# Kernel optimization log

Hardware: AMD Instinct MI355X
Metric: run time of the kernel (lower is better)

## Reference

```python
import jax, jax.numpy as jnp
import numpy as np

# ViT-B on the Lorentz hyperboloid (curvature C): points x = [x_time, x_space],
# x_time = sqrt(||x_space||^2 + C). All linear/conv/norm ops act on the space
# part and recompute time; residuals/attention-midpoints renormalize the full
# Lorentz vector back onto the hyperboloid.
B, IMG, P, CIN, D, H, L = 32, 224, 16, 3, 768, 12, 12
HD = D // H          # per-head space dim (64)
DFF = 2048           # swiglu hidden: int(2/3 * 4*768) aligned to 64
C = 1.0
EPS = 1e-6


def _time(xs):
    return jnp.sqrt(jnp.clip(jnp.sum(xs * xs, -1, keepdims=True) + C, EPS, None))


def _to_lorentz(xs):
    return jnp.concatenate([_time(xs), xs], -1)


def _project(z):
    # renormalize full Lorentz vector so <z,z>_L = -C
    zz = jnp.sum(z[..., 1:] ** 2, -1, keepdims=True) - z[..., :1] ** 2
    return z * (jnp.sqrt(C) / jnp.sqrt(jnp.clip(-zz, EPS, None)))


def _lorentz_ln(x, g, b):
    xs = x[..., 1:]
    mu = xs.mean(-1, keepdims=True)
    var = ((xs - mu) ** 2).mean(-1, keepdims=True)
    xs = (xs - mu) / jnp.sqrt(var + 1e-6) * g + b
    return _to_lorentz(xs)


def _lresnet(x, y, w):
    # Lorentzian weighted residual: midpoint of x and w*y, projected to manifold
    return _project(x + w * y)


def _rope_tables():
    # 2D axial rope over the 14x14 patch grid, identity rotation for 1 cls token
    n = IMG // P
    d4 = HD // 4
    inv = 1.0 / (100.0 ** (np.arange(d4) / d4))
    ang = np.arange(n)[:, None] * inv[None, :]            # [n, d4]
    ay = np.repeat(ang[:, None, :], n, axis=1)            # row angles
    ax = np.repeat(ang[None, :, :], n, axis=0)            # col angles
    a = np.concatenate([ay, ax], -1).reshape(n * n, HD // 2)
    cos = np.concatenate([np.ones((1, HD // 2)), np.cos(a)], 0)
    sin = np.concatenate([np.zeros((1, HD // 2)), np.sin(a)], 0)
    return jnp.asarray(cos, jnp.float32), jnp.asarray(sin, jnp.float32)


def _apply_rope(x, cos, sin):
    # x: [B,N,H,HD]; rotate consecutive pairs (complex multiply)
    xr = x.reshape(*x.shape[:-1], -1, 2)
    x0, x1 = xr[..., 0], xr[..., 1]
    c = cos[None, :, None, :]
    s = sin[None, :, None, :]
    out = jnp.stack([x0 * c - x1 * s, x0 * s + x1 * c], -1)
    return out.reshape(x.shape)


def _attention(x, Wq, Wk, Wv, Wo, cos, sin, scale):
    b, n, _ = x.shape
    xs = x[..., 1:]
    q = (xs @ Wq).reshape(b, n, H, HD)
    k = (xs @ Wk).reshape(b, n, H, HD)
    v = (xs @ Wv).reshape(b, n, H, HD)
    q = _apply_rope(q, cos, sin)
    k = _apply_rope(k, cos, sin)
    qt = _time(q)[..., 0]   # [B,N,H]
    kt = _time(k)[..., 0]
    # Lorentz inner product <q,k>_L = -q_t k_t + q_s . k_s
    inner = jnp.einsum('bnhd,bmhd->bhnm', q, k) - jnp.einsum('bnh,bmh->bhnm', qt, kt)
    attn = jax.nn.softmax((2.0 * C + 2.0 * inner) / scale, axis=-1)
    vf = jnp.concatenate([_time(v), v], -1)               # [B,M,H,HD+1]
    mid = jnp.einsum('bhnm,bmhe->bnhe', attn, vf)         # Lorentzian midpoint
    mid = _project(mid)
    out_s = mid[..., 1:].reshape(b, n, H * HD) @ Wo       # concat heads + proj
    return _to_lorentz(out_s)


def setup_inputs() -> dict:
    key = jax.random.key(0)
    ks = jax.random.split(key, 12)
    std = 0.02
    nrm = lambda k, shape: jax.random.normal(k, shape, jnp.float32) * std
    return {
        'x': jax.random.normal(ks[0], (B, CIN, IMG, IMG), jnp.float32),
        'cls_s': nrm(ks[1], (D - 1,)),
        'Wp': nrm(ks[2], (P, P, CIN + 1, D - 1)),         # HWIO conv kernel
        'ln1_g': jnp.ones((L, D - 1), jnp.float32),
        'ln1_b': jnp.zeros((L, D - 1), jnp.float32),
        'Wq': nrm(ks[3], (L, D - 1, H * HD)),
        'Wk': nrm(ks[4], (L, D - 1, H * HD)),
        'Wv': nrm(ks[5], (L, D - 1, H * HD)),
        'Wo': nrm(ks[6], (L, H * HD, D - 1)),
        'ln2_g': jnp.ones((L, D - 1), jnp.float32),
        'ln2_b': jnp.zeros((L, D - 1), jnp.float32),
        'W1': nrm(ks[7], (L, D - 1, DFF)),
        'W2': nrm(ks[8], (L, D - 1, DFF)),
        'W3': nrm(ks[9], (L, DFF, D - 1)),
        'wy1': jnp.ones((L,), jnp.float32),
        'wy2': jnp.ones((L,), jnp.float32),
        'lnf_g': jnp.ones((D - 1,), jnp.float32),
        'lnf_b': jnp.zeros((D - 1,), jnp.float32),
    }


def reference(x, cls_s, Wp, ln1_g, ln1_b, Wq, Wk, Wv, Wo, ln2_g, ln2_b,
              W1, W2, W3, wy1, wy2, lnf_g, lnf_b):
    b = x.shape[0]
    xs = jnp.transpose(x, (0, 2, 3, 1))                   # BHWC
    xl = _to_lorentz(xs)                                  # pixel-wise time channel
    feat = jax.lax.conv_general_dilated(
        xl, Wp, (P, P), 'VALID',
        dimension_numbers=('NHWC', 'HWIO', 'NHWC'))       # [B,14,14,D-1]
    tok = _to_lorentz(feat).reshape(b, -1, D)             # [B,196,D]
    cls = jnp.broadcast_to(_to_lorentz(cls_s)[None, None, :], (b, 1, D))
    tok = jnp.concatenate([cls, tok], 1)                  # [B,197,D]
    cos, sin = _rope_tables()
    scale = jnp.sqrt(jnp.asarray(H * HD, jnp.float32))
    for l in range(L):
        xn = _lorentz_ln(tok, ln1_g[l], ln1_b[l])
        a = _attention(xn, Wq[l], Wk[l], Wv[l], Wo[l], cos, sin, scale)
        tok = _lresnet(tok, a, wy1[l])
        xn = _lorentz_ln(tok, ln2_g[l], ln2_b[l])
        hs = xn[..., 1:]
        m = _to_lorentz((jax.nn.silu(hs @ W1[l]) * (hs @ W2[l])) @ W3[l])
        tok = _lresnet(tok, m, wy2[l])
    return _lorentz_ln(tok, lnf_g, lnf_b)
```

## Files before the change

kernel.cpp:

```cpp
#include <hip/hip_runtime.h>
#include <hip/hip_bf16.h>

typedef __attribute__((ext_vector_type(8))) short short8;
typedef __attribute__((ext_vector_type(4))) float f32x4;
typedef _Float16 f16x8 __attribute__((ext_vector_type(8)));

#define NLAYER 12
#define NTOK   6304
#define MPAD   6400
#define CONVM  6272

#define QELE     ((size_t)384*208*64)
#define VELE     ((size_t)384*80*232)

#define WS_QKV ((size_t)2304*768)
#define WS_WO  ((size_t)768*768)
#define WS_W12 ((size_t)4096*768)
#define WS_W3  ((size_t)768*2048)

static constexpr size_t AL(size_t x){ return (x + 511) & ~(size_t)511; }
static constexpr size_t B_COS    = 0;
static constexpr size_t B_SIN    = AL(B_COS    + (size_t)197*32*4);
static constexpr size_t B_WPT    = AL(B_SIN    + (size_t)197*32*4);
static constexpr size_t B_APATCH = AL(B_WPT    + (size_t)768*1024*2);
static constexpr size_t B_WQKVT  = AL(B_APATCH + (size_t)CONVM*1024*2);
static constexpr size_t B_WOT    = AL(B_WQKVT  + WS_QKV*NLAYER*2);
static constexpr size_t B_W12T   = AL(B_WOT    + WS_WO*NLAYER*2);
static constexpr size_t B_W3T    = AL(B_W12T   + WS_W12*NLAYER*2);
static constexpr size_t B_TOK    = AL(B_W3T    + WS_W3*NLAYER*2);
static constexpr size_t B_ACTA   = AL(B_TOK    + (size_t)NTOK*768*4);
static constexpr size_t B_ACTB   = AL(B_ACTA   + (size_t)MPAD*768*2);
static constexpr size_t B_GOUT   = AL(B_ACTB   + (size_t)MPAD*2048*2);
static constexpr size_t B_QB     = AL(B_GOUT   + (size_t)MPAD*768*4);
static constexpr size_t B_KB     = AL(B_QB     + QELE*2);
static constexpr size_t B_VT     = AL(B_KB     + QELE*2);
static constexpr size_t B_QTB    = AL(B_VT     + VELE*2);
static constexpr size_t B_KTB    = AL(B_QTB    + (size_t)384*208*4);
static constexpr size_t B_END    = AL(B_KTB    + (size_t)384*208*4);

typedef __attribute__((address_space(1))) unsigned int gu32;
typedef __attribute__((address_space(3))) unsigned int lu32;
__device__ __forceinline__ void gld16(const void* g, void* l) {
  __builtin_amdgcn_global_load_lds((const gu32*)g, (lu32*)l, 16, 0, 0);
}

__device__ __forceinline__ float bsum(float v, float* red) {
  #pragma unroll
  for (int m = 32; m; m >>= 1) v += __shfl_xor(v, m, 64);
  __syncthreads();
  if ((threadIdx.x & 63) == 0) red[threadIdx.x >> 6] = v;
  __syncthreads();
  return red[0] + red[1] + red[2] + red[3];
}

__device__ __forceinline__ ushort h_us(float v) {
  _Float16 h = (_Float16)v;
  return *(ushort*)&h;
}
__device__ __forceinline__ float us_f(ushort u) {
  return (float)*(const _Float16*)&u;
}

__device__ __forceinline__ void xcd_remap(int& bx, int& by) {
  int gx = gridDim.x, gy = gridDim.y;
  int nwg = gx * gy;
  int orig = blockIdx.y * gx + blockIdx.x;
  int q = nwg >> 3, r = nwg & 7;
  int xcd = orig & 7, loc = orig >> 3;
  int wg = (xcd < r ? xcd * (q + 1) : r * (q + 1) + (xcd - r) * q) + loc;
  bx = wg / gy;
  by = wg % gy;
}

__global__ void k_rope_tab(float* __restrict__ cosb, float* __restrict__ sinb) {
  int idx = blockIdx.x * 256 + threadIdx.x;
  if (idx >= 197 * 32) return;
  int p = idx >> 5, j = idx & 31;
  float cv, sv;
  if (p == 0) { cv = 1.f; sv = 0.f; }
  else {
    int pp = p - 1;
    int iy = pp / 14, ix = pp - iy * 14;
    int pos = (j < 16) ? iy : ix;
    int f   = (j < 16) ? j  : j - 16;
    float inv = powf(100.f, -(float)f / 16.f);
    float a = (float)pos * inv;
    cv = cosf(a); sv = sinf(a);
  }
  cosb[idx] = cv; sinb[idx] = sv;
}

__device__ __forceinline__ void tpose_tile(const float* __restrict__ src, ushort* __restrict__ dst,
                                           int K, int N, int ldd, int imode, int tk, int tn) {
  __shared__ float ts[32][33];
  int t = threadIdx.x;
  int rr = t >> 3, c4 = (t & 7) * 4;
  int k0 = tk * 32, n0 = tn * 32;
  #pragma unroll
  for (int e = 0; e < 4; ++e) {
    int k = k0 + rr, n = n0 + c4 + e;
    ts[rr][c4 + e] = (k < K && n < N) ? src[(size_t)k * N + n] : 0.f;
  }
  __syncthreads();
  int c = n0 + rr;
  int drow = (imode == 0) ? c : (16 * (c >> 3) + (c & 7) + (imode == 2 ? 8 : 0));
  ushort4 o;
  #pragma unroll
  for (int e = 0; e < 4; ++e) {
    _Float16 hv = (_Float16)ts[c4 + e][rr];
    ((ushort*)&o)[e] = *(ushort*)&hv;
  }
  *(ushort4*)&dst[(size_t)drow * ldd + k0 + c4] = o;
}

__global__ __launch_bounds__(256) void k_tpose(const float* __restrict__ src, ushort* __restrict__ dst,
                                               int K, int N, int ktiles, int ldd) {
  int tk = blockIdx.x % ktiles, tn = blockIdx.x / ktiles;
  tpose_tile(src, dst, K, N, ldd, 0, tk, tn);
}

__global__ __launch_bounds__(256) void k_wprep12(const float* __restrict__ Wq, const float* __restrict__ Wk,
                                                 const float* __restrict__ Wv, const float* __restrict__ Wo,
                                                 const float* __restrict__ W1, const float* __restrict__ W2,
                                                 const float* __restrict__ W3,
                                                 ushort* __restrict__ wqkvt, ushort* __restrict__ wot,
                                                 ushort* __restrict__ w12t, ushort* __restrict__ w3t) {
  int gt = blockIdx.x;
  int l = gt / 6912;
  int tile = gt - l * 6912;
  const float* q  = Wq + (size_t)l * 767 * 768;
  const float* kk = Wk + (size_t)l * 767 * 768;
  const float* v  = Wv + (size_t)l * 767 * 768;
  const float* o  = Wo + (size_t)l * 768 * 767;
  const float* w1 = W1 + (size_t)l * 767 * 2048;
  const float* w2 = W2 + (size_t)l * 767 * 2048;
  const float* w3 = W3 + (size_t)l * 2048 * 767;
  ushort* dqkv = wqkvt + (size_t)l * WS_QKV;
  ushort* dwo  = wot   + (size_t)l * WS_WO;
  ushort* dw12 = w12t  + (size_t)l * WS_W12;
  ushort* dw3  = w3t   + (size_t)l * WS_W3;
  const float* src; ushort* dst;
  int K, N, ktiles, ldd, imode = 0, tl;
  if (tile < 2304) {
    int jb = tile / 576; tl = tile % 576;
    ktiles = 24; ldd = 768;
    if (jb == 0)      { src = q;  dst = dqkv;                 K = 767; N = 768; }
    else if (jb == 1) { src = kk; dst = dqkv + 768 * 768;     K = 767; N = 768; }
    else if (jb == 2) { src = v;  dst = dqkv + 2 * 768 * 768; K = 767; N = 768; }
    else              { src = o;  dst = dwo;                  K = 768; N = 767; }
  } else if (tile < 5376) {
    int jb = (tile - 2304) / 1536; tl = (tile - 2304) % 1536;
    ktiles = 24; ldd = 768; K = 767; N = 2048; dst = dw12;
    src = jb ? w2 : w1; imode = jb ? 2 : 1;
  } else {
    tl = tile - 5376; ktiles = 64; ldd = 2048; K = 2048; N = 767; src = w3; dst = dw3;
  }
  int tk = tl % ktiles, tn = tl / ktiles;
  tpose_tile(src, dst, K, N, ldd, imode, tk, tn);
}

__global__ __launch_bounds__(256) void k_im2col(const float* __restrict__ x, ushort* __restrict__ ap) {
  int r = blockIdx.x;
  int b = r / 196, pi = r - b * 196;
  int py = pi / 14, px = pi - py * 14;
  int t = threadIdx.x;
  int ph = t >> 4, pw = t & 15;
  int iy = py * 16 + ph, ix = px * 16 + pw;
  size_t base = ((size_t)b * 3 * 224 + iy) * 224 + ix;
  float x0 = x[base];
  float x1 = x[base + 224 * 224];
  float x2 = x[base + 2 * 224 * 224];
  float tv = sqrtf(fmaxf(x0 * x0 + x1 * x1 + x2 * x2 + 1.f, 1e-6f));
  size_t o = (size_t)r * 1024 + t * 4;
  ap[o] = h_us(tv); ap[o + 1] = h_us(x0); ap[o + 2] = h_us(x1); ap[o + 3] = h_us(x2);
}

template<int MODE>
__global__ __launch_bounds__(256) void k_gemmh(const ushort* __restrict__ A, const ushort* __restrict__ Bt,
                                               float* __restrict__ C, ushort* __restrict__ H,
                                               int N, int K) {
  __shared__ ushort sA[2][128 * 64];
  __shared__ ushort sB[2][128 * 64];
  int bx, by;
  xcd_remap(bx, by);
  int m0 = bx * 128, n0 = by * 128;
  int t = threadIdx.x;
  int w = t >> 6, l = t & 63;
  int wm = (w >> 1) * 64, wn = (w & 1) * 64;
  int lr = l & 15, hi = l >> 4;

  auto stage = [&](int k0, int buf) {
    #pragma unroll
    for (int i = 0; i < 4; ++i) {
      int fl = i * 256 + t;
      int r = fl >> 3, c = fl & 7;
      int cs = c ^ (r & 7);
      gld16(&A[(size_t)(m0 + r) * K + k0 + cs * 8], &sA[buf][fl * 8]);
      gld16(&Bt[(size_t)(n0 + r) * K + k0 + cs * 8], &sB[buf][fl * 8]);
    }
  };

  f32x4 acc[4][4] = {};
  stage(0, 0);
  __syncthreads();
  int buf = 0;
  for (int k0 = 0; k0 < K; k0 += 64) {
    if (k0 + 64 < K) stage(k0 + 64, buf ^ 1);
    f16x8 af[4][2], bfr[4][2];
    #pragma unroll
    for (int q = 0; q < 4; ++q) {
      int ra = wm + q * 16 + lr, rb = wn + q * 16 + lr;
      #pragma unroll
      for (int h = 0; h < 2; ++h) {
        af[q][h]  = *(const f16x8*)&sA[buf][ra * 64 + ((h * 4 + hi) ^ (ra & 7)) * 8];
        bfr[q][h] = *(const f16x8*)&sB[buf][rb * 64 + ((h * 4 + hi) ^ (rb & 7)) * 8];
      }
    }
    #pragma unroll
    for (int mi = 0; mi < 4; ++mi)
      #pragma unroll
      for (int ni = 0; ni < 4; ++ni) {
        acc[mi][ni] = __builtin_amdgcn_mfma_f32_16x16x32_f16(af[mi][0], bfr[ni][0], acc[mi][ni], 0, 0, 0);
        acc[mi][ni] = __builtin_amdgcn_mfma_f32_16x16x32_f16(af[mi][1], bfr[ni][1], acc[mi][ni], 0, 0, 0);
      }
    __syncthreads();
    buf ^= 1;
  }

  int rr = hi * 4, cc = lr;
  if (MODE == 1) {
    #pragma unroll
    for (int mi = 0; mi < 4; ++mi)
      #pragma unroll
      for (int ni = 0; ni < 4; ++ni) {
        int g = (n0 + wn + ni * 16) >> 4;
        #pragma unroll
        for (int j = 0; j < 4; ++j) {
          float v = acc[mi][ni][j];
          float p = __shfl_xor(v, 8);
          float u1 = (cc < 8) ? v : p;
          float u2 = (cc < 8) ? p : v;
          float hv = u1 / (1.f + __expf(-u1)) * u2;
          if (cc < 8)
            H[(size_t)(m0 + wm + mi * 16 + rr + j) * 2048 + g * 8 + cc] = h_us(hv);
        }
      }
  } else if (MODE == 3) {
    #pragma unroll
    for (int mi = 0; mi < 4; ++mi)
      #pragma unroll
      for (int ni = 0; ni < 4; ++ni)
        #pragma unroll
        for (int j = 0; j < 4; ++j)
          H[(size_t)(m0 + wm + mi * 16 + rr + j) * N + (n0 + wn + ni * 16 + cc)] = h_us(acc[mi][ni][j]);
  } else {
    #pragma unroll
    for (int mi = 0; mi < 4; ++mi)
      #pragma unroll
      for (int ni = 0; ni < 4; ++ni)
        #pragma unroll
        for (int j = 0; j < 4; ++j)
          C[(size_t)(m0 + wm + mi * 16 + rr + j) * N + (n0 + wn + ni * 16 + cc)] = acc[mi][ni][j];
  }
}

template<int MODE>
__global__ __launch_bounds__(512, 2) void k_g256(const ushort* __restrict__ A, const ushort* __restrict__ Bt,
                                                 ushort* __restrict__ H, int N, int K,
                                                 ushort* __restrict__ qbuf, ushort* __restrict__ kbuf,
                                                 ushort* __restrict__ vtb,
                                                 float* __restrict__ qtb, float* __restrict__ ktb,
                                                 const float* __restrict__ cosb, const float* __restrict__ sinb) {
  __shared__ ushort sA[2][2][256 * 32];
  __shared__ ushort sB[2][2][256 * 32];
  const int t = threadIdx.x;
  const int w = t >> 6, l = t & 63;
  const int wr = w >> 2, wc = w & 3;
  const int lr = l & 15, hi4 = l >> 4;
  int bx, by;
  xcd_remap(bx, by);
  const int m0 = bx * 256, n0 = by * 256;

  auto stageA = [&](int kt, int kh, int buf) {
    #pragma unroll
    for (int ii = 0; ii < 2; ++ii) {
      int q = ii * 512 + t;
      int r = q >> 2, ci = q & 3;
      gld16(&A[(size_t)(m0 + r) * K + kt * 64 + kh * 32 + ((ci ^ ((r >> 1) & 3)) * 8)], &sA[buf][kh][q * 8]);
    }
  };
  auto stageB = [&](int kt, int kh, int buf) {
    #pragma unroll
    for (int ii = 0; ii < 2; ++ii) {
      int q = ii * 512 + t;
      int r = q >> 2, ci = q & 3;
      gld16(&Bt[(size_t)(n0 + r) * K + kt * 64 + kh * 32 + ((ci ^ ((r >> 1) & 3)) * 8)], &sB[buf][kh][q * 8]);
    }
  };

  f32x4 acc[8][4] = {};
  auto ldA = [&](int buf, int ks, int G, f16x8* fr) {
    #pragma unroll
    for (int mi = 0; mi < 4; ++mi) {
      int r = wr * 128 + (G * 4 + mi) * 16 + lr;
      fr[mi] = *(const f16x8*)&sA[buf][ks][(r * 4 + (hi4 ^ ((r >> 1) & 3))) * 8];
    }
  };
  auto ldB = [&](int buf, int ks, f16x8* fr) {
    #pragma unroll
    for (int ni = 0; ni < 4; ++ni) {
      int r = wc * 64 + ni * 16 + lr;
      fr[ni] = *(const f16x8*)&sB[buf][ks][(r * 4 + (hi4 ^ ((r >> 1) & 3))) * 8];
    }
  };
  auto mmaG = [&](int G, f16x8* a, f16x8* b) {
    __builtin_amdgcn_s_setprio(1);
    #pragma unroll
    for (int mi = 0; mi < 4; ++mi)
      #pragma unroll
      for (int ni = 0; ni < 4; ++ni)
        acc[G * 4 + mi][ni] = __builtin_amdgcn_mfma_f32_16x16x32_f16(a[mi], b[ni], acc[G * 4 + mi][ni], 0, 0, 0);
    __builtin_amdgcn_s_setprio(0);
  };

  const int NT = K >> 6;
  const int NI = NT >> 1;
  stageA(0, 0, 0); stageB(0, 0, 0); stageA(0, 1, 0); stageB(0, 1, 0);

  for (int i = 0; i < NI; ++i) {
    const int T1 = 2 * i + 1, T2 = 2 * i + 2;
    const bool last = (i == NI - 1);
    f16x8 a0[4], a1[4], b0[4], b1[4];
    asm volatile("s_waitcnt vmcnt(4)" ::: "memory");
    __builtin_amdgcn_sched_barrier(0);
    __builtin_amdgcn_s_barrier();
    ldA(0, 0, 0, a0); ldB(0, 0, b0);
    stageA(T1, 0, 1);
    mmaG(0, a0, b0);
    ldA(0, 0, 1, a1);
    stageB(T1, 0, 1);
    mmaG(1, a1, b0);
    asm volatile("s_waitcnt vmcnt(4)" ::: "memory");
    __builtin_amdgcn_sched_barrier(0);
    __builtin_amdgcn_s_barrier();
    ldA(0, 1, 0, a0); ldB(0, 1, b1);
    stageA(T1, 1, 1);
    mmaG(0, a0, b1);
    ldA(0, 1, 1, a1);
    stageB(T1, 1, 1);
    mmaG(1, a1, b1);
    asm volatile("s_waitcnt vmcnt(4)" ::: "memory");
    __builtin_amdgcn_sched_barrier(0);
    __builtin_amdgcn_s_barrier();
    ldA(1, 0, 0, a0); ldB(1, 0, b0);
    if (!last) stageA(T2, 0, 0);
    mmaG(0, a0, b0);
    ldA(1, 0, 1, a1);
    if (!last) stageB(T2, 0, 0);
    mmaG(1, a1, b0);
    if (last) { asm volatile("s_waitcnt vmcnt(0)" ::: "memory"); }
    else      { asm volatile("s_waitcnt vmcnt(4)" ::: "memory"); }
    __builtin_amdgcn_sched_barrier(0);
    __builtin_amdgcn_s_barrier();
    ldA(1, 1, 0, a0); ldB(1, 1, b1);
    if (!last) stageA(T2, 1, 0);
    mmaG(0, a0, b1);
    ldA(1, 1, 1, a1);
    if (!last) stageB(T2, 1, 0);
    mmaG(1, a1, b1);
  }

  if (MODE == 2) {
    int secBase = n0 + wc * 64;
    int sec = secBase / 768;
    int hh = (secBase - sec * 768) >> 6;
    #pragma unroll
    for (int mi = 0; mi < 8; ++mi) {
      float nrm[4];
      #pragma unroll
      for (int j = 0; j < 4; ++j) {
        float ss = 0.f;
        #pragma unroll
        for (int ni = 0; ni < 4; ++ni) ss += acc[mi][ni][j] * acc[mi][ni][j];
        #pragma unroll
        for (int m = 8; m; m >>= 1) ss += __shfl_xor(ss, m, 64);
        nrm[j] = sqrtf(fmaxf(ss + 1.f, 1e-6f));
      }
      #pragma unroll
      for (int j = 0; j < 4; ++j) {
        int m = m0 + wr * 128 + mi * 16 + hi4 * 4 + j;
        if (m < NTOK) {
          int b = m / 197, nn = m - b * 197;
          int bh = b * 12 + hh;
          if (sec == 2) {
            size_t vo = (size_t)bh * 80 * 232;
            if (lr == 0) vtb[vo + nn] = h_us(nrm[j]);
            #pragma unroll
            for (int ni = 0; ni < 4; ++ni) {
              int e = ni * 16 + lr;
              vtb[vo + (size_t)(1 + e) * 232 + nn] = h_us(acc[mi][ni][j]);
            }
          } else {
            float* tb = (sec == 0) ? qtb : ktb;
            ushort* ob = (sec == 0) ? qbuf : kbuf;
            if (lr == 0) tb[(size_t)bh * 208 + nn] = nrm[j];
            size_t rowb = ((size_t)bh * 208 + nn) * 64;
            #pragma unroll
            for (int ni = 0; ni < 4; ++ni) {
              int d = ni * 16 + lr;
              float v = acc[mi][ni][j];
              float p = __shfl_xor(v, 1);
              int j2 = d >> 1;
              float cz = cosb[nn * 32 + j2], sz = sinb[nn * 32 + j2];
              float rv = ((lr & 1) == 0) ? (v * cz - p * sz) : (p * sz + v * cz);
              ob[rowb + d] = h_us(rv);
            }
          }
        }
      }
    }
  }
}

__global__ __launch_bounds__(256) void k_build_tok(const float* __restrict__ feat, const float* __restrict__ cls,
                                                   float* __restrict__ tok) {
  __shared__ float red[8];
  int r = blockIdx.x;
  int b = r / 197, i = r - b * 197;
  int t = threadIdx.x;
  const float* src = (i == 0) ? cls : (feat + (size_t)(b * 196 + i - 1) * 768);
  float v0 = src[t], v1 = src[256 + t], v2 = (t < 255) ? src[512 + t] : 0.f;
  float qs = bsum(v0 * v0 + v1 * v1 + v2 * v2, red);
  float* tp = tok + (size_t)r * 768;
  if (t == 0) tp[0] = sqrtf(fmaxf(qs + 1.f, 1e-6f));
  tp[1 + t] = v0; tp[257 + t] = v1; if (t < 255) tp[513 + t] = v2;
}

__global__ __launch_bounds__(256) void k_ln(const float* __restrict__ tok, const float* __restrict__ g,
                                            const float* __restrict__ bb, ushort* __restrict__ out) {
  __shared__ float red[8];
  int r = blockIdx.x, t = threadIdx.x;
  const float* xp = tok + (size_t)r * 768;
  float v0 = xp[1 + t], v1 = xp[257 + t], v2 = (t < 255) ? xp[513 + t] : 0.f;
  float s = bsum(v0 + v1 + v2, red);
  float q = bsum(v0 * v0 + v1 * v1 + v2 * v2, red);
  float mu = s * (1.f / 767.f);
  float rstd = rsqrtf(fmaxf(q * (1.f / 767.f) - mu * mu, 0.f) + 1e-6f);
  size_t o = (size_t)r * 768;
  out[o + t]       = h_us((v0 - mu) * rstd * g[t]       + bb[t]);
  out[o + 256 + t] = h_us((v1 - mu) * rstd * g[256 + t] + bb[256 + t]);
  if (t < 255)
    out[o + 512 + t] = h_us((v2 - mu) * rstd * g[512 + t] + bb[512 + t]);
  if (t == 255) out[o + 767] = 0;
}

__global__ __launch_bounds__(128) void k_attn(const ushort* __restrict__ qbuf,
                                              const float* __restrict__ qtb,
                                              const ushort* __restrict__ kbuf,
                                              const float* __restrict__ ktb,
                                              const ushort* __restrict__ vtb,
                                              ushort* __restrict__ outa) {
  __shared__ ushort sP[2][16 * 248];
  int bxt = blockIdx.x, bh = blockIdx.y;
  int b = bh / 12, hd = bh - b * 12;
  int t = threadIdx.x, w = t >> 6, l = t & 63;
  int rt = bxt * 2 + w;
  if (rt >= 13) return;
  int lr = l & 15, hi4 = l >> 4;
  const ushort* qg = qbuf + (size_t)bh * 208 * 64;
  const ushort* kg = kbuf + (size_t)bh * 208 * 64;
  const ushort* vg = vtb + (size_t)bh * 80 * 232;
  const float*  ktp = ktb + (size_t)bh * 208;
  const float invs = 0.03608439182435161f;
  ushort* pw = &sP[w][0];

  int qrow = (rt * 16 + lr) * 64 + hi4 * 8;
  f16x8 q0 = *(const f16x8*)&qg[qrow];
  f16x8 q1 = *(const f16x8*)&qg[qrow + 32];
  float qt4[4];
  #pragma unroll
  for (int j = 0; j < 4; ++j) qt4[j] = qtb[(size_t)bh * 208 + rt * 16 + hi4 * 4 + j];
  f32x4 acc[13];
  #pragma unroll
  for (int nt = 0; nt < 13; ++nt) {
    int kr = (nt * 16 + lr) * 64 + hi4 * 8;
    f16x8 k0 = *(const f16x8*)&kg[kr];
    f16x8 k1 = *(const f16x8*)&kg[kr + 32];
    acc[nt] = (f32x4){0.f, 0.f, 0.f, 0.f};
    acc[nt] = __builtin_amdgcn_mfma_f32_16x16x32_f16(q0, k0, acc[nt], 0, 0, 0);
    acc[nt] = __builtin_amdgcn_mfma_f32_16x16x32_f16(q1, k1, acc[nt], 0, 0, 0);
  }
  float mx[4] = {-1e30f, -1e30f, -1e30f, -1e30f};
  #pragma unroll
  for (int nt = 0; nt < 13; ++nt) {
    int cI = nt * 16 + lr;
    float ktc = ktp[cI];
    bool valid = (cI < 197);
    #pragma unroll
    for (int j = 0; j < 4; ++j) {
      float s = (2.f + 2.f * (acc[nt][j] - qt4[j] * ktc)) * invs;
      acc[nt][j] = s;
      if (valid) mx[j] = fmaxf(mx[j], s);
    }
  }
  #pragma unroll
  for (int j = 0; j < 4; ++j)
    #pragma unroll
    for (int m = 8; m; m >>= 1) mx[j] = fmaxf(mx[j], __shfl_xor(mx[j], m, 64));
  #pragma unroll
  for (int nt = 0; nt < 14; ++nt) {
    int cI = nt * 16 + lr;
    #pragma unroll
    for (int j = 0; j < 4; ++j) {
      float p = (nt < 13 && cI < 197) ? __expf(acc[nt][j] - mx[j]) : 0.f;
      pw[(hi4 * 4 + j) * 248 + cI] = h_us(p);
    }
  }
  f32x4 accO[5];
  #pragma unroll
  for (int et = 0; et < 5; ++et) accO[et] = (f32x4){0.f, 0.f, 0.f, 0.f};
  #pragma unroll
  for (int ks = 0; ks < 7; ++ks) {
    f16x8 pa = *(const f16x8*)&pw[lr * 248 + ks * 32 + hi4 * 8];
    #pragma unroll
    for (int et = 0; et < 5; ++et) {
      int er = et * 16 + lr;
      f16x8 bv = *(const f16x8*)&vg[(er > 64 ? 64 : er) * 232 + ks * 32 + hi4 * 8];
      accO[et] = __builtin_amdgcn_mfma_f32_16x16x32_f16(pa, bv, accO[et], 0, 0, 0);
    }
  }
  float ssq[4] = {0.f, 0.f, 0.f, 0.f};
  #pragma unroll
  for (int et = 0; et < 4; ++et)
    #pragma unroll
    for (int j = 0; j < 4; ++j) ssq[j] += accO[et][j] * accO[et][j];
  if (lr == 0) {
    #pragma unroll
    for (int j = 0; j < 4; ++j) ssq[j] += accO[4][j] * accO[4][j];
  }
  #pragma unroll
  for (int j = 0; j < 4; ++j)
    #pragma unroll
    for (int m = 8; m; m >>= 1) ssq[j] += __shfl_xor(ssq[j], m, 64);
  float rf4[4];
  #pragma unroll
  for (int j = 0; j < 4; ++j) {
    float o0 = __shfl(accO[0][j], (l & 48));
    rf4[j] = rsqrtf(fmaxf(2.f * o0 * o0 - ssq[j], 1e-6f));
  }
  #pragma unroll
  for (int et = 0; et < 5; ++et) {
    int e = et * 16 + lr;
    if (e == 0 || e >= 65) continue;
    #pragma unroll
    for (int j = 0; j < 4; ++j) {
      int n = rt * 16 + hi4 * 4 + j;
      if (n < 197)
        outa[((size_t)(b * 197 + n)) * 768 + hd * 64 + (e - 1)] = h_us(accO[et][j] * rf4[j]);
    }
  }
}

template<int FIN>
__global__ __launch_bounds__(256) void k_resnet_ln(float* __restrict__ tok, const ushort* __restrict__ s,
                                                   const float* __restrict__ wyp, int l,
                                                   const float* __restrict__ g, const float* __restrict__ bb,
                                                   ushort* __restrict__ out16, float* __restrict__ out32) {
  __shared__ float red[8];
  __shared__ float bc[1];
  int r = blockIdx.x, t = threadIdx.x;
  float w = wyp[l];
  const ushort* sp = s + (size_t)r * 768;
  float* tp = tok + (size_t)r * 768;
  float s0 = us_f(sp[t]), s1 = us_f(sp[256 + t]), s2 = (t < 255) ? us_f(sp[512 + t]) : 0.f;
  float qs = bsum(s0 * s0 + s1 * s1 + s2 * s2, red);
  float at = sqrtf(fmaxf(qs + 1.f, 1e-6f));
  float z0 = tp[1 + t] + w * s0;
  float z1 = tp[257 + t] + w * s1;
  float z2 = (t < 255) ? (tp[513 + t] + w * s2) : 0.f;
  float zs = bsum(z0 * z0 + z1 * z1 + z2 * z2, red);
  if (t == 0) bc[0] = tp[0] + w * at;
  __syncthreads();
  float zt = bc[0];
  float rf = rsqrtf(fmaxf(zt * zt - zs, 1e-6f));
  float n0 = z0 * rf, n1 = z1 * rf, n2 = z2 * rf;
  tp[1 + t] = n0; tp[257 + t] = n1; if (t < 255) tp[513 + t] = n2;
  if (t == 0) tp[0] = zt * rf;
  float sm = bsum(n0 + n1 + n2, red);
  float sq = bsum(n0 * n0 + n1 * n1 + n2 * n2, red);
  float mu = sm * (1.f / 767.f);
  float rstd = rsqrtf(fmaxf(sq * (1.f / 767.f) - mu * mu, 0.f) + 1e-6f);
  float y0 = (n0 - mu) * rstd * g[t] + bb[t];
  float y1 = (n1 - mu) * rstd * g[256 + t] + bb[256 + t];
  float y2 = (t < 255) ? ((n2 - mu) * rstd * g[512 + t] + bb[512 + t]) : 0.f;
  if (FIN) {
    float qq = bsum(y0 * y0 + y1 * y1 + y2 * y2, red);
    float* op = out32 + (size_t)r * 768;
    op[1 + t] = y0; op[257 + t] = y1; if (t < 255) op[513 + t] = y2;
    if (t == 0) op[0] = sqrtf(fmaxf(qq + 1.f, 1e-6f));
  } else {
    size_t o = (size_t)r * 768;
    out16[o + t] = h_us(y0);
    out16[o + 256 + t] = h_us(y1);
    if (t < 255) out16[o + 512 + t] = h_us(y2);
    if (t == 255) out16[o + 767] = 0;
  }
}

extern "C" void kernel_launch(void* const* d_in, const int* in_sizes, int n_in,
                              void* d_out, int out_size, void* d_ws, size_t ws_size,
                              hipStream_t stream) {
  const float* x     = (const float*)d_in[0];
  const float* cls_s = (const float*)d_in[1];
  const float* Wp    = (const float*)d_in[2];
  const float* ln1g  = (const float*)d_in[3];
  const float* ln1b  = (const float*)d_in[4];
  const float* Wq    = (const float*)d_in[5];
  const float* Wk    = (const float*)d_in[6];
  const float* Wv    = (const float*)d_in[7];
  const float* Wo    = (const float*)d_in[8];
  const float* ln2g  = (const float*)d_in[9];
  const float* ln2b  = (const float*)d_in[10];
  const float* W1    = (const float*)d_in[11];
  const float* W2    = (const float*)d_in[12];
  const float* W3    = (const float*)d_in[13];
  const float* wy1   = (const float*)d_in[14];
  const float* wy2   = (const float*)d_in[15];
  const float* lnfg  = (const float*)d_in[16];
  const float* lnfb  = (const float*)d_in[17];

  if (ws_size < B_END) return;

  char* ws = (char*)d_ws;
  float*  cosb   = (float*)(ws + B_COS);
  float*  sinb   = (float*)(ws + B_SIN);
  ushort* wpt    = (ushort*)(ws + B_WPT);
  ushort* apatch = (ushort*)(ws + B_APATCH);
  ushort* wqkvt  = (ushort*)(ws + B_WQKVT);
  ushort* wot    = (ushort*)(ws + B_WOT);
  ushort* w12t   = (ushort*)(ws + B_W12T);
  ushort* w3t    = (ushort*)(ws + B_W3T);
  float*  tok    = (float*)(ws + B_TOK);
  ushort* acta   = (ushort*)(ws + B_ACTA);
  ushort* actb   = (ushort*)(ws + B_ACTB);
  float*  gout   = (float*)(ws + B_GOUT);
  ushort* gouth  = (ushort*)(ws + B_GOUT);
  ushort* qbuf   = (ushort*)(ws + B_QB);
  ushort* kbuf   = (ushort*)(ws + B_KB);
  ushort* vtb    = (ushort*)(ws + B_VT);
  float*  qtb    = (float*)(ws + B_QTB);
  float*  ktb    = (float*)(ws + B_KTB);

  hipMemsetAsync(vtb, 0, VELE * 2, stream);

  k_rope_tab<<<25, 256, 0, stream>>>(cosb, sinb);
  k_tpose<<<32 * 24, 256, 0, stream>>>(Wp, wpt, 1024, 767, 32, 1024);
  k_im2col<<<CONVM, 256, 0, stream>>>(x, apatch);
  k_wprep12<<<6912 * NLAYER, 256, 0, stream>>>(Wq, Wk, Wv, Wo, W1, W2, W3, wqkvt, wot, w12t, w3t);
  k_gemmh<0><<<dim3(49, 6), 256, 0, stream>>>(apatch, wpt, gout, nullptr, 768, 1024);
  k_build_tok<<<NTOK, 256, 0, stream>>>(gout, cls_s, tok);
  k_ln<<<NTOK, 256, 0, stream>>>(tok, ln1g, ln1b, acta);

  for (int l = 0; l < NLAYER; ++l) {
    const ushort* wq_l  = wqkvt + (size_t)l * WS_QKV;
    const ushort* wo_l  = wot   + (size_t)l * WS_WO;
    const ushort* w12_l = w12t  + (size_t)l * WS_W12;
    const ushort* w3_l  = w3t   + (size_t)l * WS_W3;

    k_g256<2><<<dim3(25, 9), 512, 0, stream>>>(acta, wq_l, nullptr, 2304, 768,
                                               qbuf, kbuf, vtb, qtb, ktb, cosb, sinb);
    k_attn<<<dim3(7, 384), 128, 0, stream>>>(qbuf, qtb, kbuf, ktb, vtb, acta);
    k_gemmh<3><<<dim3(50, 6), 256, 0, stream>>>(acta, wo_l, nullptr, gouth, 768, 768);
    k_resnet_ln<0><<<NTOK, 256, 0, stream>>>(tok, gouth, wy1, l,
                                             ln2g + (size_t)l * 767, ln2b + (size_t)l * 767, acta, nullptr);

    k_gemmh<1><<<dim3(50, 32), 256, 0, stream>>>(acta, w12_l, nullptr, actb, 4096, 768);
    k_gemmh<3><<<dim3(50, 6), 256, 0, stream>>>(actb, w3_l, nullptr, gouth, 768, 2048);
    if (l < NLAYER - 1)
      k_resnet_ln<0><<<NTOK, 256, 0, stream>>>(tok, gouth, wy2, l,
                                               ln1g + (size_t)(l + 1) * 767, ln1b + (size_t)(l + 1) * 767,
                                               acta, nullptr);
    else
      k_resnet_ln<1><<<NTOK, 256, 0, stream>>>(tok, gouth, wy2, l, lnfg, lnfb, nullptr, (float*)d_out);
  }
}
```

Baseline: 3.263 ms.

## Store residual stream in fp16, single-buffer GEMM staging, vectorize transpose loads

Moves the residual token buffer from fp32 to fp16, halving its traffic in the residual and layernorm kernels, at the cost of accumulating rounding error across layers in the residual path. Removes double buffering from the main GEMM so each K step loads, syncs, then computes. This halves LDS use and may raise occupancy, but loses overlap of global loads with MFMA work. Also vectorizes the weight transpose reads with float4 when the source is aligned.

```diff
diff --git a/kernel.cpp b/kernel.cpp
--- a/kernel.cpp
+++ b/kernel.cpp
@@ -28,7 +28,7 @@
 static constexpr size_t B_W12T   = AL(B_WOT    + WS_WO*NLAYER*2);
 static constexpr size_t B_W3T    = AL(B_W12T   + WS_W12*NLAYER*2);
 static constexpr size_t B_TOK    = AL(B_W3T    + WS_W3*NLAYER*2);
-static constexpr size_t B_ACTA   = AL(B_TOK    + (size_t)NTOK*768*4);
+static constexpr size_t B_ACTA   = AL(B_TOK    + (size_t)NTOK*768*2);
 static constexpr size_t B_ACTB   = AL(B_ACTA   + (size_t)MPAD*768*2);
 static constexpr size_t B_GOUT   = AL(B_ACTB   + (size_t)MPAD*2048*2);
 static constexpr size_t B_QB     = AL(B_GOUT   + (size_t)MPAD*768*4);
@@ -96,10 +96,17 @@
   int t = threadIdx.x;
   int rr = t >> 3, c4 = (t & 7) * 4;
   int k0 = tk * 32, n0 = tn * 32;
-  #pragma unroll
-  for (int e = 0; e < 4; ++e) {
-    int k = k0 + rr, n = n0 + c4 + e;
-    ts[rr][c4 + e] = (k < K && n < N) ? src[(size_t)k * N + n] : 0.f;
+  int k = k0 + rr, nb = n0 + c4;
+  const float* sp = src + (size_t)k * N + nb;
+  if (k < K && nb + 3 < N && (((size_t)sp & 15) == 0)) {
+    float4 v = *(const float4*)sp;
+    ts[rr][c4] = v.x; ts[rr][c4 + 1] = v.y; ts[rr][c4 + 2] = v.z; ts[rr][c4 + 3] = v.w;
+  } else {
+    #pragma unroll
+    for (int e = 0; e < 4; ++e) {
+      int n = nb + e;
+      ts[rr][c4 + e] = (k < K && n < N) ? src[(size_t)k * N + n] : 0.f;
+    }
   }
   __syncthreads();
   int c = n0 + rr;
@@ -179,8 +186,8 @@
 __global__ __launch_bounds__(256) void k_gemmh(const ushort* __restrict__ A, const ushort* __restrict__ Bt,
                                                float* __restrict__ C, ushort* __restrict__ H,
                                                int N, int K) {
-  __shared__ ushort sA[2][128 * 64];
-  __shared__ ushort sB[2][128 * 64];
+  __shared__ ushort sA[128 * 64];
+  __shared__ ushort sB[128 * 64];
   int bx, by;
   xcd_remap(bx, by);
   int m0 = bx * 128, n0 = by * 128;
@@ -188,32 +195,25 @@
   int w = t >> 6, l = t & 63;
   int wm = (w >> 1) * 64, wn = (w & 1) * 64;
   int lr = l & 15, hi = l >> 4;
-
-  auto stage = [&](int k0, int buf) {
+  f32x4 acc[4][4] = {};
+  for (int k0 = 0; k0 < K; k0 += 64) {
     #pragma unroll
     for (int i = 0; i < 4; ++i) {
       int fl = i * 256 + t;
       int r = fl >> 3, c = fl & 7;
       int cs = c ^ (r & 7);
-      gld16(&A[(size_t)(m0 + r) * K + k0 + cs * 8], &sA[buf][fl * 8]);
-      gld16(&Bt[(size_t)(n0 + r) * K + k0 + cs * 8], &sB[buf][fl * 8]);
-    }
-  };
-
-  f32x4 acc[4][4] = {};
-  stage(0, 0);
-  __syncthreads();
-  int buf = 0;
-  for (int k0 = 0; k0 < K; k0 += 64) {
-    if (k0 + 64 < K) stage(k0 + 64, buf ^ 1);
+      gld16(&A[(size_t)(m0 + r) * K + k0 + cs * 8], &sA[fl * 8]);
+      gld16(&Bt[(size_t)(n0 + r) * K + k0 + cs * 8], &sB[fl * 8]);
+    }
+    __syncthreads();
     f16x8 af[4][2], bfr[4][2];
     #pragma unroll
     for (int q = 0; q < 4; ++q) {
       int ra = wm + q * 16 + lr, rb = wn + q * 16 + lr;
       #pragma unroll
       for (int h = 0; h < 2; ++h) {
-        af[q][h]  = *(const f16x8*)&sA[buf][ra * 64 + ((h * 4 + hi) ^ (ra & 7)) * 8];
-        bfr[q][h] = *(const f16x8*)&sB[buf][rb * 64 + ((h * 4 + hi) ^ (rb & 7)) * 8];
+        af[q][h]  = *(const f16x8*)&sA[ra * 64 + ((h * 4 + hi) ^ (ra & 7)) * 8];
+        bfr[q][h] = *(const f16x8*)&sB[rb * 64 + ((h * 4 + hi) ^ (rb & 7)) * 8];
       }
     }
     #pragma unroll
@@ -224,9 +224,7 @@
         acc[mi][ni] = __builtin_amdgcn_mfma_f32_16x16x32_f16(af[mi][1], bfr[ni][1], acc[mi][ni], 0, 0, 0);
       }
     __syncthreads();
-    buf ^= 1;
-  }
-
+  }
   int rr = hi * 4, cc = lr;
   if (MODE == 1) {
     #pragma unroll
@@ -423,7 +421,7 @@
 }
 
 __global__ __launch_bounds__(256) void k_build_tok(const float* __restrict__ feat, const float* __restrict__ cls,
-                                                   float* __restrict__ tok) {
+                                                   ushort* __restrict__ tok) {
   __shared__ float red[8];
   int r = blockIdx.x;
   int b = r / 197, i = r - b * 197;
@@ -431,17 +429,17 @@
   const float* src = (i == 0) ? cls : (feat + (size_t)(b * 196 + i - 1) * 768);
   float v0 = src[t], v1 = src[256 + t], v2 = (t < 255) ? src[512 + t] : 0.f;
   float qs = bsum(v0 * v0 + v1 * v1 + v2 * v2, red);
-  float* tp = tok + (size_t)r * 768;
-  if (t == 0) tp[0] = sqrtf(fmaxf(qs + 1.f, 1e-6f));
-  tp[1 + t] = v0; tp[257 + t] = v1; if (t < 255) tp[513 + t] = v2;
-}
-
-__global__ __launch_bounds__(256) void k_ln(const float* __restrict__ tok, const float* __restrict__ g,
+  ushort* tp = tok + (size_t)r * 768;
+  if (t == 0) tp[0] = h_us(sqrtf(fmaxf(qs + 1.f, 1e-6f)));
+  tp[1 + t] = h_us(v0); tp[257 + t] = h_us(v1); if (t < 255) tp[513 + t] = h_us(v2);
+}
+
+__global__ __launch_bounds__(256) void k_ln(const ushort* __restrict__ tok, const float* __restrict__ g,
                                             const float* __restrict__ bb, ushort* __restrict__ out) {
   __shared__ float red[8];
   int r = blockIdx.x, t = threadIdx.x;
-  const float* xp = tok + (size_t)r * 768;
-  float v0 = xp[1 + t], v1 = xp[257 + t], v2 = (t < 255) ? xp[513 + t] : 0.f;
+  const ushort* xp = tok + (size_t)r * 768;
+  float v0 = us_f(xp[1 + t]), v1 = us_f(xp[257 + t]), v2 = (t < 255) ? us_f(xp[513 + t]) : 0.f;
   float s = bsum(v0 + v1 + v2, red);
   float q = bsum(v0 * v0 + v1 * v1 + v2 * v2, red);
   float mu = s * (1.f / 767.f);
@@ -562,7 +560,7 @@
 }
 
 template<int FIN>
-__global__ __launch_bounds__(256) void k_resnet_ln(float* __restrict__ tok, const ushort* __restrict__ s,
+__global__ __launch_bounds__(256) void k_resnet_ln(ushort* __restrict__ tok, const ushort* __restrict__ s,
                                                    const float* __restrict__ wyp, int l,
                                                    const float* __restrict__ g, const float* __restrict__ bb,
                                                    ushort* __restrict__ out16, float* __restrict__ out32) {
@@ -571,21 +569,21 @@
   int r = blockIdx.x, t = threadIdx.x;
   float w = wyp[l];
   const ushort* sp = s + (size_t)r * 768;
-  float* tp = tok + (size_t)r * 768;
+  ushort* tp = tok + (size_t)r * 768;
   float s0 = us_f(sp[t]), s1 = us_f(sp[256 + t]), s2 = (t < 255) ? us_f(sp[512 + t]) : 0.f;
   float qs = bsum(s0 * s0 + s1 * s1 + s2 * s2, red);
   float at = sqrtf(fmaxf(qs + 1.f, 1e-6f));
-  float z0 = tp[1 + t] + w * s0;
-  float z1 = tp[257 + t] + w * s1;
-  float z2 = (t < 255) ? (tp[513 + t] + w * s2) : 0.f;
+  float z0 = us_f(tp[1 + t]) + w * s0;
+  float z1 = us_f(tp[257 + t]) + w * s1;
+  float z2 = (t < 255) ? (us_f(tp[513 + t]) + w * s2) : 0.f;
   float zs = bsum(z0 * z0 + z1 * z1 + z2 * z2, red);
-  if (t == 0) bc[0] = tp[0] + w * at;
+  if (t == 0) bc[0] = us_f(tp[0]) + w * at;
   __syncthreads();
   float zt = bc[0];
   float rf = rsqrtf(fmaxf(zt * zt - zs, 1e-6f));
   float n0 = z0 * rf, n1 = z1 * rf, n2 = z2 * rf;
-  tp[1 + t] = n0; tp[257 + t] = n1; if (t < 255) tp[513 + t] = n2;
-  if (t == 0) tp[0] = zt * rf;
+  tp[1 + t] = h_us(n0); tp[257 + t] = h_us(n1); if (t < 255) tp[513 + t] = h_us(n2);
+  if (t == 0) tp[0] = h_us(zt * rf);
   float sm = bsum(n0 + n1 + n2, red);
   float sq = bsum(n0 * n0 + n1 * n1 + n2 * n2, red);
   float mu = sm * (1.f / 767.f);
@@ -640,7 +638,7 @@
   ushort* wot    = (ushort*)(ws + B_WOT);
   ushort* w12t   = (ushort*)(ws + B_W12T);
   ushort* w3t    = (ushort*)(ws + B_W3T);
-  float*  tok    = (float*)(ws + B_TOK);
+  ushort* tok    = (ushort*)(ws + B_TOK);
   ushort* acta   = (ushort*)(ws + B_ACTA);
   ushort* actb   = (ushort*)(ws + B_ACTB);
   float*  gout   = (float*)(ws + B_GOUT);
```

Result: no change. 3.249 ms (-0.4%).
